# Kernel optimization log

Measured on AMD Instinct MI355X. Metric: run time of the kernel, lower is better.

## Reference

```python
import jax, jax.numpy as jnp
import numpy as np

NH = 32
LN_EPS = 1e-5

def _mlp2(x, w1, b1, w2, b2):
    # Linear -> ReLU -> Linear (torch convention: y = x @ W^T + b)
    return jnp.maximum(x @ w1.T + b1, 0.0) @ w2.T + b2

def _layernorm(x, g, b):
    m = x.mean(-1, keepdims=True)
    v = jnp.mean((x - m) ** 2, axis=-1, keepdims=True)
    return (x - m) / jnp.sqrt(v + LN_EPS) * g + b

def _pos_enc(pos):
    # P[..., 2i] = sin(pos/(i+1)*pi), P[..., 2i+1] = cos(pos/(i+1)*pi)
    i = jnp.arange(NH // 2, dtype=pos.dtype)
    ang = pos[..., None] * (jnp.pi / (i + 1.0))  # [B, L, NH/2]
    return jnp.stack([jnp.sin(ang), jnp.cos(ang)], axis=-1).reshape(pos.shape[0], pos.shape[1], NH)

def _forward(x0, x1, pos0, pos1, xcT,
             e0w1, e0b1, e0w2, e0b2,
             e1w1, e1b1, e1w2, e1b2,
             ecw1, ecb1, ecw2, ecb2,
             wq, wk, wv, wo,
             ln1g, ln1b, ln2g, ln2b,
             f1w1, f1b1, f1w2, f1b2,
             f2w1, f2b1, f2w2, f2b2,
             l0, l1):
    # InputFeature
    e0 = _mlp2(x0, e0w1, e0b1, e0w2, e0b2) + _pos_enc(pos0)      # [B, l0, 32]
    e1 = _mlp2(x1, e1w1, e1b1, e1w2, e1b2) + _pos_enc(pos1)      # [B, l1, 32]
    ec = _mlp2(xcT, ecw1, ecb1, ecw2, ecb2)                      # [B, 32]
    xIn = jnp.concatenate([e0, e1, ec[:, None, :]], axis=1)      # [B, L, 32], L = l0+l1+1
    # AttentionLayer: attention over the feature axis (faithful to bmm(q^T, k))
    q = xIn @ wq.T; k = xIn @ wk.T; v = xIn @ wv.T               # [B, L, 32]
    L = xIn.shape[1]
    score = jnp.einsum('blh,blg->bhg', q, k) / jnp.sqrt(jnp.asarray(L, xIn.dtype))  # [B, 32, 32]
    att = jax.nn.softmax(score, axis=-1)
    a = jnp.einsum('bhg,blg->blh', att, v) @ wo.T                # [B, L, 32]
    # addnorm1 (dropout in eval = identity) + ffn1 + addnorm2 + ffn2
    h1 = _layernorm(a + xIn, ln1g, ln1b)
    h2 = _mlp2(h1, f1w1, f1b1, f1w2, f1b2)
    h3 = _layernorm(h2 + xIn, ln2g, ln2b)
    y = _mlp2(h3, f2w1, f2b1, f2w2, f2b2)[..., 0]                # [B, L]
    # segment-mean pooling: sum of per-segment means (last segment = xc token)
    return y[:, :l0].mean(-1) + y[:, l0:l0 + l1].mean(-1) + y[:, l0 + l1:].mean(-1)

def setup_inputs() -> dict:
    key = jax.random.key(0)
    ks = iter(jax.random.split(key, 48))
    B, L0, L1, N0, N1, NXC = 2048, 365, 366, 8, 16, 32
    lin = lambda o, i: jax.random.normal(next(ks), (o, i), jnp.float32) * np.float32(1.0 / np.sqrt(i))
    d = {}
    d['x0'] = jax.random.normal(next(ks), (B, L0, N0), jnp.float32)
    d['x1'] = jax.random.normal(next(ks), (B, L1, N1), jnp.float32)
    d['pos0'] = jax.random.uniform(next(ks), (B, L0), jnp.float32) * 365.0
    d['pos1'] = jax.random.uniform(next(ks), (B, L1), jnp.float32) * 365.0
    d['xcT'] = jax.random.normal(next(ks), (B, NXC), jnp.float32)
    d['e0w1'] = lin(NH, N0); d['e0b1'] = jnp.zeros((NH,), jnp.float32)
    d['e0w2'] = lin(NH, NH); d['e0b2'] = jnp.zeros((NH,), jnp.float32)
    d['e1w1'] = lin(NH, N1); d['e1b1'] = jnp.zeros((NH,), jnp.float32)
    d['e1w2'] = lin(NH, NH); d['e1b2'] = jnp.zeros((NH,), jnp.float32)
    d['ecw1'] = lin(NH, NXC); d['ecb1'] = jnp.zeros((NH,), jnp.float32)
    d['ecw2'] = lin(NH, NH); d['ecb2'] = jnp.zeros((NH,), jnp.float32)
    d['wq'] = lin(NH, NH); d['wk'] = lin(NH, NH); d['wv'] = lin(NH, NH); d['wo'] = lin(NH, NH)
    d['ln1g'] = jnp.ones((NH,), jnp.float32); d['ln1b'] = jnp.zeros((NH,), jnp.float32)
    d['ln2g'] = jnp.ones((NH,), jnp.float32); d['ln2b'] = jnp.zeros((NH,), jnp.float32)
    d['f1w1'] = lin(NH, NH); d['f1b1'] = jnp.zeros((NH,), jnp.float32)
    d['f1w2'] = lin(NH, NH); d['f1b2'] = jnp.zeros((NH,), jnp.float32)
    d['f2w1'] = lin(NH, NH); d['f2b1'] = jnp.zeros((NH,), jnp.float32)
    d['f2w2'] = lin(1, NH); d['f2b2'] = jnp.zeros((1,), jnp.float32)
    d['l0'] = L0; d['l1'] = L1
    return d

def reference(x0, x1, pos0, pos1, xcT,
              e0w1, e0b1, e0w2, e0b2, e1w1, e1b1, e1w2, e1b2,
              ecw1, ecb1, ecw2, ecb2, wq, wk, wv, wo,
              ln1g, ln1b, ln2g, ln2b,
              f1w1, f1b1, f1w2, f1b2, f2w1, f2b1, f2w2, f2b2,
              l0, l1):
    return _forward(x0, x1, pos0, pos1, xcT,
                    e0w1, e0b1, e0w2, e0b2, e1w1, e1b1, e1w2, e1b2,
                    ecw1, ecb1, ecw2, ecb2, wq, wk, wv, wo,
                    ln1g, ln1b, ln2g, ln2b,
                    f1w1, f1b1, f1w2, f1b2, f2w1, f2b1, f2w2, f2b2,
                    l0, l1)
```

## Files before the change

kernel.cpp:

```cpp
#include <hip/hip_runtime.h>
#include <math.h>

#define L0T 365
#define L1T 366
#define LT  732
#define NTILE 46
#define NSEG 23
#define NW   4
#define NTHR 256
#define NSLOT 12

typedef short svec8 __attribute__((ext_vector_type(8)));
typedef float fvec4 __attribute__((ext_vector_type(4)));
typedef float fvec16 __attribute__((ext_vector_type(16)));
typedef unsigned uvec4 __attribute__((ext_vector_type(4)));

__device__ __forceinline__ unsigned short f2bf(float f) {
    unsigned u = __float_as_uint(f);
    u = (u + 0x7fffu + ((u >> 16) & 1u)) >> 16;
    return (unsigned short)u;
}
__device__ __forceinline__ float bf2f(unsigned short s) {
    return __uint_as_float(((unsigned)s) << 16);
}
__device__ __forceinline__ unsigned pk2(float a, float b) {
    return (unsigned)f2bf(a) | ((unsigned)f2bf(b) << 16);
}
__device__ __forceinline__ unsigned cvtpk(float a, float b) {
    unsigned r;
    asm("v_cvt_pk_bf16_f32 %0, %1, %2" : "=v"(r) : "v"(a), "v"(b));
    return r;
}
__device__ __forceinline__ float pgetv(uvec4 p, int j) {
    unsigned u = p[j >> 1];
    return bf2f((unsigned short)((j & 1) ? (u >> 16) : (u & 0xffffu)));
}
__device__ __forceinline__ svec8 pack8(float4 a, float4 c) {
    uvec4 u;
    u[0] = cvtpk(a.x, a.y); u[1] = cvtpk(a.z, a.w);
    u[2] = cvtpk(c.x, c.y); u[3] = cvtpk(c.z, c.w);
    return __builtin_bit_cast(svec8, u);
}
__device__ __forceinline__ void fastsc(float rev, float& s, float& c) {
    float fr;
    asm("v_fract_f32 %0, %1" : "=v"(fr) : "v"(rev));
    asm("v_sin_f32 %0, %1"   : "=v"(s)  : "v"(fr));
    asm("v_cos_f32 %0, %1"   : "=v"(c)  : "v"(fr));
}

__device__ __forceinline__ void embed_pass(
    const unsigned short* __restrict__ T1,
    const unsigned short* __restrict__ T2,
    const float* __restrict__ Bh, const float* __restrict__ Bx,
    svec8 bx, int ln, int Q, float* __restrict__ out)
{
    svec8 w1f0 = *(const svec8*)&T1[ln * 8];
    svec8 w1f1 = *(const svec8*)&T1[512 + ln * 8];
    const fvec4* bh = (const fvec4*)&Bh[Q * 8];
    fvec4 d0 = __builtin_amdgcn_mfma_f32_16x16x32_bf16(w1f0, bx, bh[0], 0, 0, 0);
    fvec4 d1 = __builtin_amdgcn_mfma_f32_16x16x32_bf16(w1f1, bx, bh[1], 0, 0, 0);
    uvec4 hu;
    hu[0] = cvtpk(fmaxf(d0[0], 0.f), fmaxf(d0[1], 0.f));
    hu[1] = cvtpk(fmaxf(d0[2], 0.f), fmaxf(d0[3], 0.f));
    hu[2] = cvtpk(fmaxf(d1[0], 0.f), fmaxf(d1[1], 0.f));
    hu[3] = cvtpk(fmaxf(d1[2], 0.f), fmaxf(d1[3], 0.f));
    svec8 hf = __builtin_bit_cast(svec8, hu);
    svec8 w2f0 = *(const svec8*)&T2[ln * 8];
    svec8 w2f1 = *(const svec8*)&T2[512 + ln * 8];
    const fvec4* bb = (const fvec4*)&Bx[Q * 8];
    fvec4 g0 = __builtin_amdgcn_mfma_f32_16x16x32_bf16(w2f0, hf, bb[0], 0, 0, 0);
    fvec4 g1 = __builtin_amdgcn_mfma_f32_16x16x32_bf16(w2f1, hf, bb[1], 0, 0, 0);
    out[0] = g0[0]; out[1] = g0[1]; out[2] = g0[2]; out[3] = g0[3];
    out[4] = g1[0]; out[5] = g1[1]; out[6] = g1[2]; out[7] = g1[3];
}

__device__ __forceinline__ void load_tile(
    int t, int b, int tk, int Q,
    const float* __restrict__ x0, const float* __restrict__ x1,
    const float* __restrict__ pos0, const float* __restrict__ pos1,
    svec8& bx, float& pv, int& seg, int& tl)
{
    seg = (t >= NSEG) ? 1 : 0;
    tl  = (seg ? (t - NSEG) : t) * 16 + tk;
    const int lim = seg ? L1T : L0T;
    const bool tvalid = tl < lim;
    #pragma unroll
    for (int j = 0; j < 8; j++) bx[j] = 0;
    const bool ld = tvalid && (seg ? (Q < 2) : (Q == 0));
    if (ld) {
        const float4* px = seg
            ? (const float4*)(x1 + ((size_t)b * L1T + tl) * 16 + Q * 8)
            : (const float4*)(x0 + ((size_t)b * L0T + tl) * 8);
        bx = pack8(px[0], px[1]);
    }
    pv = 0.f;
    if (tvalid) pv = seg ? pos1[(size_t)b * L1T + tl] : pos0[(size_t)b * L0T + tl];
}

__device__ __forceinline__ void finish_xv(
    int seg, int tl, int Q, const float* __restrict__ e, float pv, float4 pwr,
    const float* __restrict__ ECV, float* __restrict__ xv)
{
    const int lim = seg ? L1T : L0T;
    const bool tvalid = tl < lim;
    const bool isxc = seg && (tl == L1T);
    const float pwa[4] = {pwr.x, pwr.y, pwr.z, pwr.w};
    #pragma unroll
    for (int j = 0; j < 8; j += 2) {
        float s, c; fastsc(pv * pwa[j >> 1], s, c);
        float a0 = e[j] + s, a1 = e[j + 1] + c;
        xv[j]     = tvalid ? a0 : (isxc ? ECV[Q * 8 + j]     : 0.f);
        xv[j + 1] = tvalid ? a1 : (isxc ? ECV[Q * 8 + j + 1] : 0.f);
    }
}

__global__ __launch_bounds__(NTHR, 4) void fused_kernel(
    const float* __restrict__ x0,  const float* __restrict__ x1,
    const float* __restrict__ pos0,const float* __restrict__ pos1,
    const float* __restrict__ xcT,
    const float* __restrict__ e0w1,const float* __restrict__ e0b1,
    const float* __restrict__ e0w2,const float* __restrict__ e0b2,
    const float* __restrict__ e1w1,const float* __restrict__ e1b1,
    const float* __restrict__ e1w2,const float* __restrict__ e1b2,
    const float* __restrict__ ecw1,const float* __restrict__ ecb1,
    const float* __restrict__ ecw2,const float* __restrict__ ecb2,
    const float* __restrict__ wq,  const float* __restrict__ wk,
    const float* __restrict__ wv,  const float* __restrict__ wo,
    const float* __restrict__ ln1g,const float* __restrict__ ln1b,
    const float* __restrict__ ln2g,const float* __restrict__ ln2b,
    const float* __restrict__ f1w1,const float* __restrict__ f1b1,
    const float* __restrict__ f1w2,const float* __restrict__ f1b2,
    const float* __restrict__ f2w1,const float* __restrict__ f2b1,
    const float* __restrict__ f2w2,const float* __restrict__ f2b2,
    float* __restrict__ out)
{
    const int b   = blockIdx.x;
    const int tid = threadIdx.x;
    const int w   = tid >> 6;
    const int ln  = tid & 63;
    const int tk  = ln & 15;
    const int Q   = ln >> 4;
    const int Lr0 = ((tk >> 2) * 8) + (tk & 3);
    const int Lr1 = Lr0 + 4;

    __shared__ unsigned short TBL[4 * 1024] __attribute__((aligned(16)));
    __shared__ float BIA[128] __attribute__((aligned(16)));
    __shared__ unsigned PCK[128] __attribute__((aligned(16)));
    __shared__ float SCR[2048] __attribute__((aligned(16)));
    __shared__ unsigned short Wbb[1024] __attribute__((aligned(16)));
    __shared__ float ECV[32] __attribute__((aligned(16)));
    __shared__ float red[NW * 3];

    float* T1f  = SCR;
    float* CmT2 = SCR + 1024;

    float4 pwr;
    pwr.x = 0.5f / (float)(Q * 4 + 1);
    pwr.y = 0.5f / (float)(Q * 4 + 2);
    pwr.z = 0.5f / (float)(Q * 4 + 3);
    pwr.w = 0.5f / (float)(Q * 4 + 4);

    for (int idx = tid; idx < 1024; idx += NTHR) {
        int f = idx >> 9, lane = (idx >> 3) & 63, j = idx & 7;
        int tkk = lane & 15, QQ = lane >> 4;
        int Lr = ((tkk >> 2) * 8) + (tkk & 3) + f * 4;
        int col = QQ * 8 + j;
        TBL[idx]        = (col < 8)  ? f2bf(e0w1[Lr * 8  + col]) : (unsigned short)0;
        TBL[1024 + idx] = f2bf(e0w2[Lr * 32 + col]);
        TBL[2048 + idx] = (col < 16) ? f2bf(e1w1[Lr * 16 + col]) : (unsigned short)0;
        TBL[3072 + idx] = f2bf(e1w2[Lr * 32 + col]);
        CmT2[idx] = 0.f;
    }
    if (tid < 128) {
        int s = tid >> 5, i = tid & 31;
        float bv;
        if      (s == 0) bv = e0b1[i];
        else if (s == 1) bv = e0b2[i];
        else if (s == 2) bv = e1b1[i];
        else             bv = e1b2[i];
        BIA[tid] = bv;
    }
    if (tid < 128) {
        int t8 = tid >> 4, q = (tid >> 2) & 3, i = tid & 3, f = q * 8 + 2 * i;
        const float* sp;
        if      (t8 == 0) sp = ln1g;
        else if (t8 == 1) sp = ln1b;
        else if (t8 == 2) sp = ln2g;
        else if (t8 == 3) sp = ln2b;
        else if (t8 == 4) sp = f1b1;
        else if (t8 == 5) sp = f1b2;
        else if (t8 == 6) sp = f2b1;
        else              sp = f2w2;
        PCK[tid] = pk2(sp[f], sp[f + 1]);
    }
    float* ECH = T1f;
    if (tid >= 224) {
        int i = tid - 224;
        const float4* xr = (const float4*)(xcT + (size_t)b * 32);
        const float4* wr = (const float4*)&ecw1[i * 32];
        float a = ecb1[i];
        #pragma unroll
        for (int j4 = 0; j4 < 8; j4++) {
            float4 ww = wr[j4], xx = xr[j4];
            a = fmaf(ww.x, xx.x, a); a = fmaf(ww.y, xx.y, a);
            a = fmaf(ww.z, xx.z, a); a = fmaf(ww.w, xx.w, a);
        }
        ECH[i] = fmaxf(a, 0.f);
    }
    __syncthreads();
    if (tid >= 224) {
        int i = tid - 224;
        const float4* wr = (const float4*)&ecw2[i * 32];
        float a = ecb2[i];
        #pragma unroll
        for (int j4 = 0; j4 < 8; j4++) {
            float4 ww = wr[j4];
            a = fmaf(ww.x, ECH[j4 * 4 + 0], a); a = fmaf(ww.y, ECH[j4 * 4 + 1], a);
            a = fmaf(ww.z, ECH[j4 * 4 + 2], a); a = fmaf(ww.w, ECH[j4 * 4 + 3], a);
        }
        ECV[i] = a;
    }
    __syncthreads();

    uvec4 xs[NSLOT];

    {
        unsigned short* ST = (unsigned short*)T1f;
        const int feat = ln & 31, half = ln >> 5;
        fvec16 dG;
        #pragma unroll
        for (int i = 0; i < 16; i++) dG[i] = 0.f;

        #pragma unroll
        for (int s = 0; s < NSLOT; s++) {
            const int t = s * NW + w;
            if (t < NTILE) {
                svec8 bx; float pv; int sg, tl;
                load_tile(t, b, tk, Q, x0, x1, pos0, pos1, bx, pv, sg, tl);
                float e[8];
                {
                    const unsigned short* T = TBL + sg * 2048;
                    const float* Bb = BIA + sg * 64;
                    embed_pass(T, T + 1024, Bb, Bb + 32, bx, ln, Q, e);
                }
                float xv[8]; finish_xv(sg, tl, Q, e, pv, pwr, ECV, xv);
                uvec4 pk;
                pk[0] = cvtpk(xv[0], xv[1]); pk[1] = cvtpk(xv[2], xv[3]);
                pk[2] = cvtpk(xv[4], xv[5]); pk[3] = cvtpk(xv[6], xv[7]);
                xs[s] = pk;
                __builtin_amdgcn_sched_barrier(0);
                *(uvec4*)&ST[(w * 16 + tk) * 32 + Q * 8] = pk;
                __builtin_amdgcn_sched_barrier(0);
                svec8 af;
                #pragma unroll
                for (int j = 0; j < 8; j++)
                    af[j] = (short)ST[w * 512 + (half * 8 + j) * 32 + feat];
                __builtin_amdgcn_sched_barrier(0);
                dG = __builtin_amdgcn_mfma_f32_32x32x16_bf16(af, af, dG, 0, 0, 0);
            }
        }
        #pragma unroll
        for (int rg = 0; rg < 16; rg++) {
            int row = (rg & 3) + 8 * (rg >> 2) + 4 * half;
            atomicAdd(&CmT2[row * 32 + feat], dG[rg]);
        }
    }
    __syncthreads();

    for (int idx = tid; idx < 1024; idx += NTHR) {
        int i = idx >> 5, g = idx & 31;
        const float4* cr = (const float4*)&CmT2[i * 32];
        const float4* wr = (const float4*)&wk[g * 32];
        float a = 0.f;
        #pragma unroll
        for (int j4 = 0; j4 < 8; j4++) {
            float4 cc = cr[j4], ww = wr[j4];
            a = fmaf(cc.x, ww.x, a); a = fmaf(cc.y, ww.y, a);
            a = fmaf(cc.z, ww.z, a); a = fmaf(cc.w, ww.w, a);
        }
        T1f[idx] = a;
    }
    __syncthreads();
    const float rsL = rsqrtf((float)LT);
    for (int idx = tid; idx < 1024; idx += NTHR) {
        int h = idx >> 5, g = idx & 31;
        const float4* qr = (const float4*)&wq[h * 32];
        float a = 0.f;
        #pragma unroll
        for (int i4 = 0; i4 < 8; i4++) {
            float4 qq = qr[i4];
            a = fmaf(qq.x, T1f[(i4 * 4 + 0) * 32 + g], a);
            a = fmaf(qq.y, T1f[(i4 * 4 + 1) * 32 + g], a);
            a = fmaf(qq.z, T1f[(i4 * 4 + 2) * 32 + g], a);
            a = fmaf(qq.w, T1f[(i4 * 4 + 3) * 32 + g], a);
        }
        CmT2[idx] = a * rsL;
    }
    __syncthreads();
    {
        int r = tid >> 3, c0 = (tid & 7) * 4;
        float4 vv = *(const float4*)&CmT2[r * 32 + c0];
        float m = fmaxf(fmaxf(vv.x, vv.y), fmaxf(vv.z, vv.w));
        m = fmaxf(m, __shfl_xor(m, 1));
        m = fmaxf(m, __shfl_xor(m, 2));
        m = fmaxf(m, __shfl_xor(m, 4));
        float ex = __expf(vv.x - m), ey = __expf(vv.y - m);
        float ez = __expf(vv.z - m), ew = __expf(vv.w - m);
        float s = ex + ey + ez + ew;
        s += __shfl_xor(s, 1); s += __shfl_xor(s, 2); s += __shfl_xor(s, 4);
        float inv = 1.f / s;
        float4 o; o.x = ex * inv; o.y = ey * inv; o.z = ez * inv; o.w = ew * inv;
        *(float4*)&CmT2[r * 32 + c0] = o;
    }
    __syncthreads();
    for (int idx = tid; idx < 1024; idx += NTHR) {
        int h = idx >> 5, j = idx & 31;
        const float4* pr = (const float4*)&CmT2[h * 32];
        float a = 0.f;
        #pragma unroll
        for (int g4 = 0; g4 < 8; g4++) {
            float4 pp = pr[g4];
            a = fmaf(pp.x, wv[(g4 * 4 + 0) * 32 + j], a);
            a = fmaf(pp.y, wv[(g4 * 4 + 1) * 32 + j], a);
            a = fmaf(pp.z, wv[(g4 * 4 + 2) * 32 + j], a);
            a = fmaf(pp.w, wv[(g4 * 4 + 3) * 32 + j], a);
        }
        T1f[idx] = a;
    }
    __syncthreads();
    for (int idx = tid; idx < 1024; idx += NTHR) {
        int o = idx >> 5, j = idx & 31;
        const float4* orow = (const float4*)&wo[o * 32];
        float a = 0.f;
        #pragma unroll
        for (int h4 = 0; h4 < 8; h4++) {
            float4 oo = orow[h4];
            a = fmaf(oo.x, T1f[(h4 * 4 + 0) * 32 + j], a);
            a = fmaf(oo.y, T1f[(h4 * 4 + 1) * 32 + j], a);
            a = fmaf(oo.z, T1f[(h4 * 4 + 2) * 32 + j], a);
            a = fmaf(oo.w, T1f[(h4 * 4 + 3) * 32 + j], a);
        }
        Wbb[idx] = f2bf(a + (o == j ? 1.f : 0.f));
    }
    __syncthreads();

    svec8 wbf0 = *(const svec8*)&Wbb[Lr0 * 32 + Q * 8];
    svec8 wbf1 = *(const svec8*)&Wbb[Lr1 * 32 + Q * 8];
    svec8 a1f0, a1f1, a2f0, a2f1, a3f0, a3f1;
    #pragma unroll
    for (int j = 0; j < 8; j++) {
        a1f0[j] = (short)f2bf(f1w1[Lr0 * 32 + Q * 8 + j]);
        a1f1[j] = (short)f2bf(f1w1[Lr1 * 32 + Q * 8 + j]);
        a2f0[j] = (short)f2bf(f1w2[Lr0 * 32 + Q * 8 + j]);
        a2f1[j] = (short)f2bf(f1w2[Lr1 * 32 + Q * 8 + j]);
        a3f0[j] = (short)f2bf(f2w1[Lr0 * 32 + Q * 8 + j]);
        a3f1[j] = (short)f2bf(f2w1[Lr1 * 32 + Q * 8 + j]);
    }
    const float ybias = f2b2[0];
    const fvec4 zc = {0.f, 0.f, 0.f, 0.f};
    const uvec4* P4 = (const uvec4*)PCK;

    float s0 = 0.f, s1 = 0.f, s2 = 0.f;
    #pragma unroll
    for (int s = 0; s < NSLOT; s++) {
        const int t = s * NW + w;
        if (t < NTILE) {
            const uvec4 px = xs[s];
            svec8 bx = __builtin_bit_cast(svec8, px);
            float xf[8];
            #pragma unroll
            for (int j = 0; j < 8; j++) xf[j] = pgetv(px, j);

            fvec4 d0 = __builtin_amdgcn_mfma_f32_16x16x32_bf16(wbf0, bx, zc, 0, 0, 0);
            fvec4 d1 = __builtin_amdgcn_mfma_f32_16x16x32_bf16(wbf1, bx, zc, 0, 0, 0);
            float v[8];
            #pragma unroll
            for (int j = 0; j < 4; j++) { v[j] = d0[j]; v[4 + j] = d1[j]; }
            float S = 0.f, Sq = 0.f;
            #pragma unroll
            for (int j = 0; j < 8; j++) { S += v[j]; Sq = fmaf(v[j], v[j], Sq); }
            S  += __shfl_xor(S, 16);  Sq += __shfl_xor(Sq, 16);
            S  += __shfl_xor(S, 32);  Sq += __shfl_xor(Sq, 32);
            float mean = S * (1.f / 32.f);
            float var = fmaxf(Sq * (1.f / 32.f) - mean * mean, 0.f);
            float rs = rsqrtf(var + 1e-5f);
            uvec4 pg1 = P4[Q], pb1 = P4[4 + Q];
            float n[8];
            #pragma unroll
            for (int j = 0; j < 8; j++)
                n[j] = (v[j] - mean) * rs * pgetv(pg1, j) + pgetv(pb1, j);
            uvec4 tu;
            tu[0] = cvtpk(n[0], n[1]); tu[1] = cvtpk(n[2], n[3]);
            tu[2] = cvtpk(n[4], n[5]); tu[3] = cvtpk(n[6], n[7]);
            svec8 tf = __builtin_bit_cast(svec8, tu);
            fvec4 u0 = __builtin_amdgcn_mfma_f32_16x16x32_bf16(a1f0, tf, zc, 0, 0, 0);
            fvec4 u1 = __builtin_amdgcn_mfma_f32_16x16x32_bf16(a1f1, tf, zc, 0, 0, 0);
            uvec4 pc1 = P4[16 + Q];
            uvec4 uu;
            uu[0] = cvtpk(fmaxf(u0[0] + pgetv(pc1, 0), 0.f), fmaxf(u0[1] + pgetv(pc1, 1), 0.f));
            uu[1] = cvtpk(fmaxf(u0[2] + pgetv(pc1, 2), 0.f), fmaxf(u0[3] + pgetv(pc1, 3), 0.f));
            uu[2] = cvtpk(fmaxf(u1[0] + pgetv(pc1, 4), 0.f), fmaxf(u1[1] + pgetv(pc1, 5), 0.f));
            uu[3] = cvtpk(fmaxf(u1[2] + pgetv(pc1, 6), 0.f), fmaxf(u1[3] + pgetv(pc1, 7), 0.f));
            svec8 uf = __builtin_bit_cast(svec8, uu);
            fvec4 g0 = __builtin_amdgcn_mfma_f32_16x16x32_bf16(a2f0, uf, zc, 0, 0, 0);
            fvec4 g1 = __builtin_amdgcn_mfma_f32_16x16x32_bf16(a2f1, uf, zc, 0, 0, 0);
            uvec4 pc2 = P4[20 + Q];
            #pragma unroll
            for (int j = 0; j < 8; j++)
                v[j] = (j < 4 ? g0[j] : g1[j - 4]) + pgetv(pc2, j) + xf[j];
            float S2 = 0.f, Sq2 = 0.f;
            #pragma unroll
            for (int j = 0; j < 8; j++) { S2 += v[j]; Sq2 = fmaf(v[j], v[j], Sq2); }
            S2  += __shfl_xor(S2, 16);  Sq2 += __shfl_xor(Sq2, 16);
            S2  += __shfl_xor(S2, 32);  Sq2 += __shfl_xor(Sq2, 32);
            float mean2 = S2 * (1.f / 32.f);
            float var2 = fmaxf(Sq2 * (1.f / 32.f) - mean2 * mean2, 0.f);
            float rs2 = rsqrtf(var2 + 1e-5f);
            uvec4 pg2 = P4[8 + Q], pb2 = P4[12 + Q];
            float n2[8];
            #pragma unroll
            for (int j = 0; j < 8; j++)
                n2[j] = (v[j] - mean2) * rs2 * pgetv(pg2, j) + pgetv(pb2, j);
            uvec4 t2u;
            t2u[0] = cvtpk(n2[0], n2[1]); t2u[1] = cvtpk(n2[2], n2[3]);
            t2u[2] = cvtpk(n2[4], n2[5]); t2u[3] = cvtpk(n2[6], n2[7]);
            svec8 t2 = __builtin_bit_cast(svec8, t2u);
            fvec4 q0 = __builtin_amdgcn_mfma_f32_16x16x32_bf16(a3f0, t2, zc, 0, 0, 0);
            fvec4 q1 = __builtin_amdgcn_mfma_f32_16x16x32_bf16(a3f1, t2, zc, 0, 0, 0);
            uvec4 pc3 = P4[24 + Q], pw2 = P4[28 + Q];
            float yp = 0.f;
            #pragma unroll
            for (int j = 0; j < 8; j++) {
                float e = (j < 4 ? q0[j] : q1[j - 4]) + pgetv(pc3, j);
                yp = fmaf(pgetv(pw2, j), fmaxf(e, 0.f), yp);
            }
            yp += __shfl_xor(yp, 16); yp += __shfl_xor(yp, 32);
            if (Q == 0) {
                const int sg = (t >= NSEG) ? 1 : 0;
                const int tl = (sg ? (t - NSEG) : t) * 16 + tk;
                float yv = yp + ybias;
                if (sg == 0) { if (tl < L0T) s0 += yv; }
                else {
                    if (tl < L1T)       s1 += yv;
                    else if (tl == L1T) s2 += yv;
                }
            }
        }
    }

    s0 += __shfl_xor(s0, 1); s0 += __shfl_xor(s0, 2);
    s0 += __shfl_xor(s0, 4); s0 += __shfl_xor(s0, 8);
    s1 += __shfl_xor(s1, 1); s1 += __shfl_xor(s1, 2);
    s1 += __shfl_xor(s1, 4); s1 += __shfl_xor(s1, 8);
    s2 += __shfl_xor(s2, 1); s2 += __shfl_xor(s2, 2);
    s2 += __shfl_xor(s2, 4); s2 += __shfl_xor(s2, 8);
    if (ln == 0) { red[w * 3] = s0; red[w * 3 + 1] = s1; red[w * 3 + 2] = s2; }
    __syncthreads();
    if (tid == 0) {
        float a0 = 0.f, a1 = 0.f, a2 = 0.f;
        #pragma unroll
        for (int k = 0; k < NW; k++) {
            a0 += red[k * 3]; a1 += red[k * 3 + 1]; a2 += red[k * 3 + 2];
        }
        out[b] = a0 / (float)L0T + a1 / (float)L1T + a2;
    }
}

extern "C" void kernel_launch(void* const* d_in, const int* in_sizes, int n_in,
                              void* d_out, int out_size, void* d_ws, size_t ws_size,
                              hipStream_t stream)
{
    const float* x0   = (const float*)d_in[0];
    const float* x1   = (const float*)d_in[1];
    const float* pos0 = (const float*)d_in[2];
    const float* pos1 = (const float*)d_in[3];
    const float* xcT  = (const float*)d_in[4];
    const float* e0w1 = (const float*)d_in[5];
    const float* e0b1 = (const float*)d_in[6];
    const float* e0w2 = (const float*)d_in[7];
    const float* e0b2 = (const float*)d_in[8];
    const float* e1w1 = (const float*)d_in[9];
    const float* e1b1 = (const float*)d_in[10];
    const float* e1w2 = (const float*)d_in[11];
    const float* e1b2 = (const float*)d_in[12];
    const float* ecw1 = (const float*)d_in[13];
    const float* ecb1 = (const float*)d_in[14];
    const float* ecw2 = (const float*)d_in[15];
    const float* ecb2 = (const float*)d_in[16];
    const float* wq   = (const float*)d_in[17];
    const float* wk   = (const float*)d_in[18];
    const float* wv   = (const float*)d_in[19];
    const float* wo   = (const float*)d_in[20];
    const float* ln1g = (const float*)d_in[21];
    const float* ln1b = (const float*)d_in[22];
    const float* ln2g = (const float*)d_in[23];
    const float* ln2b = (const float*)d_in[24];
    const float* f1w1 = (const float*)d_in[25];
    const float* f1b1 = (const float*)d_in[26];
    const float* f1w2 = (const float*)d_in[27];
    const float* f1b2 = (const float*)d_in[28];
    const float* f2w1 = (const float*)d_in[29];
    const float* f2b1 = (const float*)d_in[30];
    const float* f2w2 = (const float*)d_in[31];
    const float* f2b2 = (const float*)d_in[32];
    float* out = (float*)d_out;

    const int B = in_sizes[0] / (L0T * 8);

    hipLaunchKernelGGL(fused_kernel, dim3(B), dim3(NTHR), 0, stream,
                       x0, x1, pos0, pos1, xcT,
                       e0w1, e0b1, e0w2, e0b2, e1w1, e1b1, e1w2, e1b2,
                       ecw1, ecb1, ecw2, ecb2, wq, wk, wv, wo,
                       ln1g, ln1b, ln2g, ln2b,
                       f1w1, f1b1, f1w2, f1b2, f2w1, f2b1, f2w2, f2b2,
                       out);
}
```

Before: 327.2 us.

## Split fused kernel into gram and pipeline kernels, recomputing embeddings

The single fused kernel, which kept all per-tile embeddings in registers (xs[12]) between the Gram/attention phase and the FFN phase, becomes two kernels. The first computes embeddings, the Gram matrix and the folded attention weight and writes them to workspace. The second recomputes the embeddings and runs the LN/FFN pipeline, with weight fragments loaded from LDS on demand instead of held in registers. This frees registers to raise launch bounds from 4 to 8 blocks per CU, at the cost of doing the embedding MLP and sin/cos twice, a second launch, and a workspace round trip.

Measured after the change: 314.2 us. -4.0%, faster.

```diff
diff --git a/kernel.cpp b/kernel.cpp
--- a/kernel.cpp
+++ b/kernel.cpp
@@ -46,6 +46,10 @@
     asm("v_fract_f32 %0, %1" : "=v"(fr) : "v"(rev));
     asm("v_sin_f32 %0, %1"   : "=v"(s)  : "v"(fr));
     asm("v_cos_f32 %0, %1"   : "=v"(c)  : "v"(fr));
+}
+__device__ __forceinline__ svec8 ldfrag(const unsigned short* p) {
+    asm volatile("" : "+v"(p));
+    return *(const svec8*)p;
 }
 
 __device__ __forceinline__ void embed_pass(
@@ -114,7 +118,7 @@
     }
 }
 
-__global__ __launch_bounds__(NTHR, 4) void fused_kernel(
+__global__ __launch_bounds__(NTHR, 8) void embed_gram_kernel(
     const float* __restrict__ x0,  const float* __restrict__ x1,
     const float* __restrict__ pos0,const float* __restrict__ pos1,
     const float* __restrict__ xcT,
@@ -126,13 +130,7 @@
     const float* __restrict__ ecw2,const float* __restrict__ ecb2,
     const float* __restrict__ wq,  const float* __restrict__ wk,
     const float* __restrict__ wv,  const float* __restrict__ wo,
-    const float* __restrict__ ln1g,const float* __restrict__ ln1b,
-    const float* __restrict__ ln2g,const float* __restrict__ ln2b,
-    const float* __restrict__ f1w1,const float* __restrict__ f1b1,
-    const float* __restrict__ f1w2,const float* __restrict__ f1b2,
-    const float* __restrict__ f2w1,const float* __restrict__ f2b1,
-    const float* __restrict__ f2w2,const float* __restrict__ f2b2,
-    float* __restrict__ out)
+    unsigned short* __restrict__ wsWb, float* __restrict__ wsEC)
 {
     const int b   = blockIdx.x;
     const int tid = threadIdx.x;
@@ -140,16 +138,11 @@
     const int ln  = tid & 63;
     const int tk  = ln & 15;
     const int Q   = ln >> 4;
-    const int Lr0 = ((tk >> 2) * 8) + (tk & 3);
-    const int Lr1 = Lr0 + 4;
 
     __shared__ unsigned short TBL[4 * 1024] __attribute__((aligned(16)));
     __shared__ float BIA[128] __attribute__((aligned(16)));
-    __shared__ unsigned PCK[128] __attribute__((aligned(16)));
     __shared__ float SCR[2048] __attribute__((aligned(16)));
-    __shared__ unsigned short Wbb[1024] __attribute__((aligned(16)));
     __shared__ float ECV[32] __attribute__((aligned(16)));
-    __shared__ float red[NW * 3];
 
     float* T1f  = SCR;
     float* CmT2 = SCR + 1024;
@@ -180,19 +173,6 @@
         else             bv = e1b2[i];
         BIA[tid] = bv;
     }
-    if (tid < 128) {
-        int t8 = tid >> 4, q = (tid >> 2) & 3, i = tid & 3, f = q * 8 + 2 * i;
-        const float* sp;
-        if      (t8 == 0) sp = ln1g;
-        else if (t8 == 1) sp = ln1b;
-        else if (t8 == 2) sp = ln2g;
-        else if (t8 == 3) sp = ln2b;
-        else if (t8 == 4) sp = f1b1;
-        else if (t8 == 5) sp = f1b2;
-        else if (t8 == 6) sp = f2b1;
-        else              sp = f2w2;
-        PCK[tid] = pk2(sp[f], sp[f + 1]);
-    }
     float* ECH = T1f;
     if (tid >= 224) {
         int i = tid - 224;
@@ -219,10 +199,9 @@
             a = fmaf(ww.z, ECH[j4 * 4 + 2], a); a = fmaf(ww.w, ECH[j4 * 4 + 3], a);
         }
         ECV[i] = a;
-    }
-    __syncthreads();
-
-    uvec4 xs[NSLOT];
+        wsEC[(size_t)b * 32 + i] = a;
+    }
+    __syncthreads();
 
     {
         unsigned short* ST = (unsigned short*)T1f;
@@ -230,34 +209,28 @@
         fvec16 dG;
         #pragma unroll
         for (int i = 0; i < 16; i++) dG[i] = 0.f;
-
-        #pragma unroll
-        for (int s = 0; s < NSLOT; s++) {
-            const int t = s * NW + w;
-            if (t < NTILE) {
-                svec8 bx; float pv; int sg, tl;
-                load_tile(t, b, tk, Q, x0, x1, pos0, pos1, bx, pv, sg, tl);
-                float e[8];
-                {
-                    const unsigned short* T = TBL + sg * 2048;
-                    const float* Bb = BIA + sg * 64;
-                    embed_pass(T, T + 1024, Bb, Bb + 32, bx, ln, Q, e);
-                }
-                float xv[8]; finish_xv(sg, tl, Q, e, pv, pwr, ECV, xv);
-                uvec4 pk;
-                pk[0] = cvtpk(xv[0], xv[1]); pk[1] = cvtpk(xv[2], xv[3]);
-                pk[2] = cvtpk(xv[4], xv[5]); pk[3] = cvtpk(xv[6], xv[7]);
-                xs[s] = pk;
-                __builtin_amdgcn_sched_barrier(0);
-                *(uvec4*)&ST[(w * 16 + tk) * 32 + Q * 8] = pk;
-                __builtin_amdgcn_sched_barrier(0);
-                svec8 af;
-                #pragma unroll
-                for (int j = 0; j < 8; j++)
-                    af[j] = (short)ST[w * 512 + (half * 8 + j) * 32 + feat];
-                __builtin_amdgcn_sched_barrier(0);
-                dG = __builtin_amdgcn_mfma_f32_32x32x16_bf16(af, af, dG, 0, 0, 0);
+        for (int t = w; t < NTILE; t += NW) {
+            svec8 bx; float pv; int sg, tl;
+            load_tile(t, b, tk, Q, x0, x1, pos0, pos1, bx, pv, sg, tl);
+            float e[8];
+            {
+                const unsigned short* T = TBL + sg * 2048;
+                const float* Bb = BIA + sg * 64;
+                embed_pass(T, T + 1024, Bb, Bb + 32, bx, ln, Q, e);
             }
+            float xv[8]; finish_xv(sg, tl, Q, e, pv, pwr, ECV, xv);
+            uvec4 pk;
+            pk[0] = cvtpk(xv[0], xv[1]); pk[1] = cvtpk(xv[2], xv[3]);
+            pk[2] = cvtpk(xv[4], xv[5]); pk[3] = cvtpk(xv[6], xv[7]);
+            __builtin_amdgcn_sched_barrier(0);
+            *(uvec4*)&ST[(w * 16 + tk) * 32 + Q * 8] = pk;
+            __builtin_amdgcn_sched_barrier(0);
+            svec8 af;
+            #pragma unroll
+            for (int j = 0; j < 8; j++)
+                af[j] = (short)ST[w * 512 + (half * 8 + j) * 32 + feat];
+            __builtin_amdgcn_sched_barrier(0);
+            dG = __builtin_amdgcn_mfma_f32_32x32x16_bf16(af, af, dG, 0, 0, 0);
         }
         #pragma unroll
         for (int rg = 0; rg < 16; rg++) {
@@ -340,110 +313,192 @@
             a = fmaf(oo.z, T1f[(h4 * 4 + 2) * 32 + j], a);
             a = fmaf(oo.w, T1f[(h4 * 4 + 3) * 32 + j], a);
         }
-        Wbb[idx] = f2bf(a + (o == j ? 1.f : 0.f));
-    }
-    __syncthreads();
-
-    svec8 wbf0 = *(const svec8*)&Wbb[Lr0 * 32 + Q * 8];
-    svec8 wbf1 = *(const svec8*)&Wbb[Lr1 * 32 + Q * 8];
-    svec8 a1f0, a1f1, a2f0, a2f1, a3f0, a3f1;
-    #pragma unroll
-    for (int j = 0; j < 8; j++) {
-        a1f0[j] = (short)f2bf(f1w1[Lr0 * 32 + Q * 8 + j]);
-        a1f1[j] = (short)f2bf(f1w1[Lr1 * 32 + Q * 8 + j]);
-        a2f0[j] = (short)f2bf(f1w2[Lr0 * 32 + Q * 8 + j]);
-        a2f1[j] = (short)f2bf(f1w2[Lr1 * 32 + Q * 8 + j]);
-        a3f0[j] = (short)f2bf(f2w1[Lr0 * 32 + Q * 8 + j]);
-        a3f1[j] = (short)f2bf(f2w1[Lr1 * 32 + Q * 8 + j]);
-    }
+        wsWb[(size_t)b * 1024 + idx] = f2bf(a + (o == j ? 1.f : 0.f));
+    }
+}
+
+__global__ __launch_bounds__(NTHR, 8) void pipeline_kernel(
+    const float* __restrict__ x0,  const float* __restrict__ x1,
+    const float* __restrict__ pos0,const float* __restrict__ pos1,
+    const float* __restrict__ e0w1,const float* __restrict__ e0b1,
+    const float* __restrict__ e0w2,const float* __restrict__ e0b2,
+    const float* __restrict__ e1w1,const float* __restrict__ e1b1,
+    const float* __restrict__ e1w2,const float* __restrict__ e1b2,
+    const float* __restrict__ ln1g,const float* __restrict__ ln1b,
+    const float* __restrict__ ln2g,const float* __restrict__ ln2b,
+    const float* __restrict__ f1w1,const float* __restrict__ f1b1,
+    const float* __restrict__ f1w2,const float* __restrict__ f1b2,
+    const float* __restrict__ f2w1,const float* __restrict__ f2b1,
+    const float* __restrict__ f2w2,const float* __restrict__ f2b2,
+    const unsigned short* __restrict__ wsWb, const float* __restrict__ wsEC,
+    float* __restrict__ out)
+{
+    const int b   = blockIdx.x;
+    const int tid = threadIdx.x;
+    const int w   = tid >> 6;
+    const int ln  = tid & 63;
+    const int tk  = ln & 15;
+    const int Q   = ln >> 4;
+
+    __shared__ unsigned short TBL[4 * 1024] __attribute__((aligned(16)));
+    __shared__ unsigned short WTB[4 * 1024] __attribute__((aligned(16)));
+    __shared__ float BIA[128] __attribute__((aligned(16)));
+    __shared__ unsigned PCK[128] __attribute__((aligned(16)));
+    __shared__ float ECV[32] __attribute__((aligned(16)));
+    __shared__ float red[NW * 3];
+
+    float4 pwr;
+    pwr.x = 0.5f / (float)(Q * 4 + 1);
+    pwr.y = 0.5f / (float)(Q * 4 + 2);
+    pwr.z = 0.5f / (float)(Q * 4 + 3);
+    pwr.w = 0.5f / (float)(Q * 4 + 4);
+
+    for (int idx = tid; idx < 1024; idx += NTHR) {
+        int f = idx >> 9, lane = (idx >> 3) & 63, j = idx & 7;
+        int tkk = lane & 15, QQ = lane >> 4;
+        int Lr = ((tkk >> 2) * 8) + (tkk & 3) + f * 4;
+        int col = QQ * 8 + j;
+        TBL[idx]        = (col < 8)  ? f2bf(e0w1[Lr * 8  + col]) : (unsigned short)0;
+        TBL[1024 + idx] = f2bf(e0w2[Lr * 32 + col]);
+        TBL[2048 + idx] = (col < 16) ? f2bf(e1w1[Lr * 16 + col]) : (unsigned short)0;
+        TBL[3072 + idx] = f2bf(e1w2[Lr * 32 + col]);
+    }
+    for (int idx = tid; idx < 4096; idx += NTHR) {
+        int f = idx >> 9, lane = (idx >> 3) & 63, j = idx & 7;
+        int tkk = lane & 15, QQ = lane >> 4;
+        int Lr = ((tkk >> 2) * 8) + (tkk & 3) + (f & 1) * 4;
+        int col = QQ * 8 + j;
+        int wsel = f >> 1;
+        unsigned short vbf;
+        if      (wsel == 0) vbf = wsWb[(size_t)b * 1024 + Lr * 32 + col];
+        else if (wsel == 1) vbf = f2bf(f1w1[Lr * 32 + col]);
+        else if (wsel == 2) vbf = f2bf(f1w2[Lr * 32 + col]);
+        else                vbf = f2bf(f2w1[Lr * 32 + col]);
+        WTB[idx] = vbf;
+    }
+    if (tid < 128) {
+        int s = tid >> 5, i = tid & 31;
+        float bv;
+        if      (s == 0) bv = e0b1[i];
+        else if (s == 1) bv = e0b2[i];
+        else if (s == 2) bv = e1b1[i];
+        else             bv = e1b2[i];
+        BIA[tid] = bv;
+    }
+    if (tid < 128) {
+        int t8 = tid >> 4, q = (tid >> 2) & 3, i = tid & 3, f = q * 8 + 2 * i;
+        const float* sp;
+        if      (t8 == 0) sp = ln1g;
+        else if (t8 == 1) sp = ln1b;
+        else if (t8 == 2) sp = ln2g;
+        else if (t8 == 3) sp = ln2b;
+        else if (t8 == 4) sp = f1b1;
+        else if (t8 == 5) sp = f1b2;
+        else if (t8 == 6) sp = f2b1;
+        else              sp = f2w2;
+        PCK[tid] = pk2(sp[f], sp[f + 1]);
+    }
+    if (tid < 32) ECV[tid] = wsEC[(size_t)b * 32 + tid];
+    __syncthreads();
+
     const float ybias = f2b2[0];
     const fvec4 zc = {0.f, 0.f, 0.f, 0.f};
     const uvec4* P4 = (const uvec4*)PCK;
 
     float s0 = 0.f, s1 = 0.f, s2 = 0.f;
-    #pragma unroll
-    for (int s = 0; s < NSLOT; s++) {
-        const int t = s * NW + w;
-        if (t < NTILE) {
-            const uvec4 px = xs[s];
-            svec8 bx = __builtin_bit_cast(svec8, px);
-            float xf[8];
-            #pragma unroll
-            for (int j = 0; j < 8; j++) xf[j] = pgetv(px, j);
-
-            fvec4 d0 = __builtin_amdgcn_mfma_f32_16x16x32_bf16(wbf0, bx, zc, 0, 0, 0);
-            fvec4 d1 = __builtin_amdgcn_mfma_f32_16x16x32_bf16(wbf1, bx, zc, 0, 0, 0);
-            float v[8];
-            #pragma unroll
-            for (int j = 0; j < 4; j++) { v[j] = d0[j]; v[4 + j] = d1[j]; }
-            float S = 0.f, Sq = 0.f;
-            #pragma unroll
-            for (int j = 0; j < 8; j++) { S += v[j]; Sq = fmaf(v[j], v[j], Sq); }
-            S  += __shfl_xor(S, 16);  Sq += __shfl_xor(Sq, 16);
-            S  += __shfl_xor(S, 32);  Sq += __shfl_xor(Sq, 32);
-            float mean = S * (1.f / 32.f);
-            float var = fmaxf(Sq * (1.f / 32.f) - mean * mean, 0.f);
-            float rs = rsqrtf(var + 1e-5f);
-            uvec4 pg1 = P4[Q], pb1 = P4[4 + Q];
-            float n[8];
-            #pragma unroll
-            for (int j = 0; j < 8; j++)
-                n[j] = (v[j] - mean) * rs * pgetv(pg1, j) + pgetv(pb1, j);
-            uvec4 tu;
-            tu[0] = cvtpk(n[0], n[1]); tu[1] = cvtpk(n[2], n[3]);
-            tu[2] = cvtpk(n[4], n[5]); tu[3] = cvtpk(n[6], n[7]);
-            svec8 tf = __builtin_bit_cast(svec8, tu);
-            fvec4 u0 = __builtin_amdgcn_mfma_f32_16x16x32_bf16(a1f0, tf, zc, 0, 0, 0);
-            fvec4 u1 = __builtin_amdgcn_mfma_f32_16x16x32_bf16(a1f1, tf, zc, 0, 0, 0);
-            uvec4 pc1 = P4[16 + Q];
-            uvec4 uu;
-            uu[0] = cvtpk(fmaxf(u0[0] + pgetv(pc1, 0), 0.f), fmaxf(u0[1] + pgetv(pc1, 1), 0.f));
-            uu[1] = cvtpk(fmaxf(u0[2] + pgetv(pc1, 2), 0.f), fmaxf(u0[3] + pgetv(pc1, 3), 0.f));
-            uu[2] = cvtpk(fmaxf(u1[0] + pgetv(pc1, 4), 0.f), fmaxf(u1[1] + pgetv(pc1, 5), 0.f));
-            uu[3] = cvtpk(fmaxf(u1[2] + pgetv(pc1, 6), 0.f), fmaxf(u1[3] + pgetv(pc1, 7), 0.f));
-            svec8 uf = __builtin_bit_cast(svec8, uu);
-            fvec4 g0 = __builtin_amdgcn_mfma_f32_16x16x32_bf16(a2f0, uf, zc, 0, 0, 0);
-            fvec4 g1 = __builtin_amdgcn_mfma_f32_16x16x32_bf16(a2f1, uf, zc, 0, 0, 0);
-            uvec4 pc2 = P4[20 + Q];
-            #pragma unroll
-            for (int j = 0; j < 8; j++)
-                v[j] = (j < 4 ? g0[j] : g1[j - 4]) + pgetv(pc2, j) + xf[j];
-            float S2 = 0.f, Sq2 = 0.f;
-            #pragma unroll
-            for (int j = 0; j < 8; j++) { S2 += v[j]; Sq2 = fmaf(v[j], v[j], Sq2); }
-            S2  += __shfl_xor(S2, 16);  Sq2 += __shfl_xor(Sq2, 16);
-            S2  += __shfl_xor(S2, 32);  Sq2 += __shfl_xor(Sq2, 32);
-            float mean2 = S2 * (1.f / 32.f);
-            float var2 = fmaxf(Sq2 * (1.f / 32.f) - mean2 * mean2, 0.f);
-            float rs2 = rsqrtf(var2 + 1e-5f);
-            uvec4 pg2 = P4[8 + Q], pb2 = P4[12 + Q];
-            float n2[8];
-            #pragma unroll
-            for (int j = 0; j < 8; j++)
-                n2[j] = (v[j] - mean2) * rs2 * pgetv(pg2, j) + pgetv(pb2, j);
-            uvec4 t2u;
-            t2u[0] = cvtpk(n2[0], n2[1]); t2u[1] = cvtpk(n2[2], n2[3]);
-            t2u[2] = cvtpk(n2[4], n2[5]); t2u[3] = cvtpk(n2[6], n2[7]);
-            svec8 t2 = __builtin_bit_cast(svec8, t2u);
-            fvec4 q0 = __builtin_amdgcn_mfma_f32_16x16x32_bf16(a3f0, t2, zc, 0, 0, 0);
-            fvec4 q1 = __builtin_amdgcn_mfma_f32_16x16x32_bf16(a3f1, t2, zc, 0, 0, 0);
-            uvec4 pc3 = P4[24 + Q], pw2 = P4[28 + Q];
-            float yp = 0.f;
-            #pragma unroll
-            for (int j = 0; j < 8; j++) {
-                float e = (j < 4 ? q0[j] : q1[j - 4]) + pgetv(pc3, j);
-                yp = fmaf(pgetv(pw2, j), fmaxf(e, 0.f), yp);
-            }
-            yp += __shfl_xor(yp, 16); yp += __shfl_xor(yp, 32);
-            if (Q == 0) {
-                const int sg = (t >= NSEG) ? 1 : 0;
-                const int tl = (sg ? (t - NSEG) : t) * 16 + tk;
-                float yv = yp + ybias;
-                if (sg == 0) { if (tl < L0T) s0 += yv; }
-                else {
-                    if (tl < L1T)       s1 += yv;
-                    else if (tl == L1T) s2 += yv;
-                }
+    for (int t = w; t < NTILE; t += NW) {
+        svec8 bx0; float pv; int sg, tl;
+        load_tile(t, b, tk, Q, x0, x1, pos0, pos1, bx0, pv, sg, tl);
+        float e[8];
+        {
+            const unsigned short* T = TBL + sg * 2048;
+            const float* Bb = BIA + sg * 64;
+            embed_pass(T, T + 1024, Bb, Bb + 32, bx0, ln, Q, e);
+        }
+        float xv[8]; finish_xv(sg, tl, Q, e, pv, pwr, ECV, xv);
+        uvec4 pkx;
+        pkx[0] = cvtpk(xv[0], xv[1]); pkx[1] = cvtpk(xv[2], xv[3]);
+        pkx[2] = cvtpk(xv[4], xv[5]); pkx[3] = cvtpk(xv[6], xv[7]);
+        svec8 bx = __builtin_bit_cast(svec8, pkx);
+
+        svec8 wb0 = ldfrag(&WTB[ln * 8]);
+        svec8 wb1 = ldfrag(&WTB[512 + ln * 8]);
+        fvec4 d0 = __builtin_amdgcn_mfma_f32_16x16x32_bf16(wb0, bx, zc, 0, 0, 0);
+        fvec4 d1 = __builtin_amdgcn_mfma_f32_16x16x32_bf16(wb1, bx, zc, 0, 0, 0);
+        float v[8];
+        #pragma unroll
+        for (int j = 0; j < 4; j++) { v[j] = d0[j]; v[4 + j] = d1[j]; }
+        float S = 0.f, Sq = 0.f;
+        #pragma unroll
+        for (int j = 0; j < 8; j++) { S += v[j]; Sq = fmaf(v[j], v[j], Sq); }
+        S  += __shfl_xor(S, 16);  Sq += __shfl_xor(Sq, 16);
+        S  += __shfl_xor(S, 32);  Sq += __shfl_xor(Sq, 32);
+        float mean = S * (1.f / 32.f);
+        float var = fmaxf(Sq * (1.f / 32.f) - mean * mean, 0.f);
+        float rs = rsqrtf(var + 1e-5f);
+        uvec4 pg1 = P4[Q], pb1 = P4[4 + Q];
+        float n[8];
+        #pragma unroll
+        for (int j = 0; j < 8; j++)
+            n[j] = (v[j] - mean) * rs * pgetv(pg1, j) + pgetv(pb1, j);
+        uvec4 tu;
+        tu[0] = cvtpk(n[0], n[1]); tu[1] = cvtpk(n[2], n[3]);
+        tu[2] = cvtpk(n[4], n[5]); tu[3] = cvtpk(n[6], n[7]);
+        svec8 tf = __builtin_bit_cast(svec8, tu);
+        svec8 a1f0 = ldfrag(&WTB[1024 + ln * 8]);
+        svec8 a1f1 = ldfrag(&WTB[1536 + ln * 8]);
+        fvec4 u0 = __builtin_amdgcn_mfma_f32_16x16x32_bf16(a1f0, tf, zc, 0, 0, 0);
+        fvec4 u1 = __builtin_amdgcn_mfma_f32_16x16x32_bf16(a1f1, tf, zc, 0, 0, 0);
+        uvec4 pc1 = P4[16 + Q];
+        uvec4 uu;
+        uu[0] = cvtpk(fmaxf(u0[0] + pgetv(pc1, 0), 0.f), fmaxf(u0[1] + pgetv(pc1, 1), 0.f));
+        uu[1] = cvtpk(fmaxf(u0[2] + pgetv(pc1, 2), 0.f), fmaxf(u0[3] + pgetv(pc1, 3), 0.f));
+        uu[2] = cvtpk(fmaxf(u1[0] + pgetv(pc1, 4), 0.f), fmaxf(u1[1] + pgetv(pc1, 5), 0.f));
+        uu[3] = cvtpk(fmaxf(u1[2] + pgetv(pc1, 6), 0.f), fmaxf(u1[3] + pgetv(pc1, 7), 0.f));
+        svec8 uf = __builtin_bit_cast(svec8, uu);
+        svec8 a2f0 = ldfrag(&WTB[2048 + ln * 8]);
+        svec8 a2f1 = ldfrag(&WTB[2560 + ln * 8]);
+        fvec4 g0 = __builtin_amdgcn_mfma_f32_16x16x32_bf16(a2f0, uf, zc, 0, 0, 0);
+        fvec4 g1 = __builtin_amdgcn_mfma_f32_16x16x32_bf16(a2f1, uf, zc, 0, 0, 0);
+        uvec4 pc2 = P4[20 + Q];
+        #pragma unroll
+        for (int j = 0; j < 8; j++)
+            v[j] = (j < 4 ? g0[j] : g1[j - 4]) + pgetv(pc2, j) + xv[j];
+        float S2 = 0.f, Sq2 = 0.f;
+        #pragma unroll
+        for (int j = 0; j < 8; j++) { S2 += v[j]; Sq2 = fmaf(v[j], v[j], Sq2); }
+        S2  += __shfl_xor(S2, 16);  Sq2 += __shfl_xor(Sq2, 16);
+        S2  += __shfl_xor(S2, 32);  Sq2 += __shfl_xor(Sq2, 32);
+        float mean2 = S2 * (1.f / 32.f);
+        float var2 = fmaxf(Sq2 * (1.f / 32.f) - mean2 * mean2, 0.f);
+        float rs2 = rsqrtf(var2 + 1e-5f);
+        uvec4 pg2 = P4[8 + Q], pb2 = P4[12 + Q];
+        float n2[8];
+        #pragma unroll
+        for (int j = 0; j < 8; j++)
+            n2[j] = (v[j] - mean2) * rs2 * pgetv(pg2, j) + pgetv(pb2, j);
+        uvec4 t2u;
+        t2u[0] = cvtpk(n2[0], n2[1]); t2u[1] = cvtpk(n2[2], n2[3]);
+        t2u[2] = cvtpk(n2[4], n2[5]); t2u[3] = cvtpk(n2[6], n2[7]);
+        svec8 t2 = __builtin_bit_cast(svec8, t2u);
+        svec8 a3f0 = ldfrag(&WTB[3072 + ln * 8]);
+        svec8 a3f1 = ldfrag(&WTB[3584 + ln * 8]);
+        fvec4 q0 = __builtin_amdgcn_mfma_f32_16x16x32_bf16(a3f0, t2, zc, 0, 0, 0);
+        fvec4 q1 = __builtin_amdgcn_mfma_f32_16x16x32_bf16(a3f1, t2, zc, 0, 0, 0);
+        uvec4 pc3 = P4[24 + Q], pw2 = P4[28 + Q];
+        float yp = 0.f;
+        #pragma unroll
+        for (int j = 0; j < 8; j++) {
+            float ee = (j < 4 ? q0[j] : q1[j - 4]) + pgetv(pc3, j);
+            yp = fmaf(pgetv(pw2, j), fmaxf(ee, 0.f), yp);
+        }
+        yp += __shfl_xor(yp, 16); yp += __shfl_xor(yp, 32);
+        if (Q == 0) {
+            float yv = yp + ybias;
+            if (sg == 0) { if (tl < L0T) s0 += yv; }
+            else {
+                if (tl < L1T)       s1 += yv;
+                else if (tl == L1T) s2 += yv;
             }
         }
     }
@@ -507,11 +562,18 @@
 
     const int B = in_sizes[0] / (L0T * 8);
 
-    hipLaunchKernelGGL(fused_kernel, dim3(B), dim3(NTHR), 0, stream,
+    unsigned short* wsWb = (unsigned short*)d_ws;
+    float* wsEC = (float*)((char*)d_ws + (size_t)B * 1024 * 2);
+
+    hipLaunchKernelGGL(embed_gram_kernel, dim3(B), dim3(NTHR), 0, stream,
                        x0, x1, pos0, pos1, xcT,
                        e0w1, e0b1, e0w2, e0b2, e1w1, e1b1, e1w2, e1b2,
                        ecw1, ecb1, ecw2, ecb2, wq, wk, wv, wo,
+                       wsWb, wsEC);
+    hipLaunchKernelGGL(pipeline_kernel, dim3(B), dim3(NTHR), 0, stream,
+                       x0, x1, pos0, pos1,
+                       e0w1, e0b1, e0w2, e0b2, e1w1, e1b1, e1w2, e1b2,
                        ln1g, ln1b, ln2g, ln2b,
                        f1w1, f1b1, f1w2, f1b2, f2w1, f2b1, f2w2, f2b2,
-                       out);
-}
+                       wsWb, wsEC, out);
+}
```
